# Kernel tuning notes

Measured on AMD Instinct MI355X. Metric: run time of the kernel, lower is better.

The kernel has to match this reference:

```python
import jax, jax.numpy as jnp
import numpy as np

B, N, C = 4, 4096, 64
TARGET = 560.0          # target_size
MIN_BOX = 5.0           # min_box_size
IOU_THR = 0.2
CONF_THR = 0.001
BOX_CONF_THR = 0.01
MAX_WH = 4096.0         # class-offset trick for class-aware NMS (YOLO-style)


def setup_inputs() -> dict:
    key = jax.random.key(0)
    k1, k2, k3, k4 = jax.random.split(key, 4)
    # proposals as xyxy boxes inside the (560,560) image, realistic sizes
    cxcy = jax.random.uniform(k1, (B, N, 2), dtype=jnp.float32) * TARGET
    wh = jax.random.uniform(k2, (B, N, 2), dtype=jnp.float32) * 100.0 + 2.0
    boxes = jnp.concatenate([cxcy - wh / 2, cxcy + wh / 2], axis=-1)  # [B,N,4]
    box_scores = jax.random.uniform(k3, (B, N), dtype=jnp.float32)    # objectness/10
    cls_preds = jax.random.uniform(k4, (B, N, C), dtype=jnp.float32)  # classifier scores
    return {"boxes": boxes, "box_scores": box_scores, "cls_preds": cls_preds}


def _pairwise_iou(b):
    # b: [N,4] xyxy -> [N,N] IoU
    area = (b[:, 2] - b[:, 0]) * (b[:, 3] - b[:, 1])
    lt = jnp.maximum(b[:, None, :2], b[None, :, :2])
    rb = jnp.minimum(b[:, None, 2:], b[None, :, 2:])
    wh = jnp.clip(rb - lt, 0.0)
    inter = wh[..., 0] * wh[..., 1]
    return inter / (area[:, None] + area[None, :] - inter + 1e-9)


def _detect_single(boxes, box_scores, cls_preds):
    # --- filter_boxes: clip to image, drop tiny boxes and low objectness ---
    b = jnp.clip(boxes, 0.0, TARGET)                       # [N,4]
    w = b[:, 2] - b[:, 0]
    h = b[:, 3] - b[:, 1]
    # YOLO-style combined confidence: objectness * per-class score
    cls_conf = cls_preds * box_scores[:, None]             # [N,C]
    conf = jnp.max(cls_conf, axis=-1)                      # [N]
    cls = jnp.argmax(cls_conf, axis=-1)                    # [N] int
    valid = ((box_scores > BOX_CONF_THR) & (w > MIN_BOX) & (h > MIN_BOX)
             & (conf > CONF_THR))
    # --- sort by confidence, descending (invalid boxes sink to bottom) ---
    score_key = jnp.where(valid, conf, -1.0)
    order = jnp.argsort(-score_key)
    b = b[order]; conf = conf[order]; cls = cls[order]; v = valid[order]
    # --- class-aware greedy NMS via per-class coordinate offset ---
    ob = b + (cls.astype(b.dtype) * MAX_WH)[:, None]
    iou = _pairwise_iou(ob)                                # [N,N]
    n = b.shape[0]
    idx = jnp.arange(n)

    def body(suppressed, i):
        keep_i = v[i] & (~suppressed[i])
        new_sup = suppressed | (keep_i & (iou[i] > IOU_THR) & (idx > i))
        return new_sup, keep_i

    _, keeps = jax.lax.scan(body, jnp.zeros(n, dtype=bool), idx)
    keep = (keeps & v).astype(b.dtype)                     # [N]
    det = jnp.concatenate([b, conf[:, None], cls.astype(b.dtype)[:, None]], -1)
    return det * keep[:, None]                             # [N,6] padded with zeros


def reference(boxes, box_scores, cls_preds):
    # [B,N,6]: (x1,y1,x2,y2,conf,class) per kept detection, zero rows otherwise
    return jax.vmap(_detect_single)(boxes, box_scores, cls_preds)
```

## Files before the change

kernel.cpp:

```cpp
#include <hip/hip_runtime.h>
#include <stdint.h>

#pragma clang fp contract(off)

typedef unsigned long long u64;
typedef unsigned int u32;
typedef unsigned short u16;

namespace {
constexpr int BB = 4;
constexpr int NN = 4096;
constexpr int CC = 64;
constexpr int BN = BB * NN;
constexpr float TARGET = 560.0f;
constexpr float MIN_BOX = 5.0f;
constexpr float IOU_THR = 0.2f;
constexpr float CONF_THR = 0.001f;
constexpr float BOX_CONF_THR = 0.01f;
constexpr float MAX_WH = 4096.0f;
constexpr int MAXB = 1024;
}

__device__ __forceinline__ void zero_row(float* __restrict__ out, int p) {
    float2* o2 = (float2*)(out + (size_t)p * 6);
    float2 z; z.x = 0.0f; z.y = 0.0f;
    o2[0] = z; o2[1] = z; o2[2] = z;
}

__device__ __forceinline__ void emit_row(float* __restrict__ out, int p,
                                         float4 bc, float cf, float cls) {
    float2* o2 = (float2*)(out + (size_t)p * 6);
    float2 aa; aa.x = bc.x; aa.y = bc.y;
    float2 cc; cc.x = bc.z; cc.y = bc.w;
    float2 ee; ee.x = cf;   ee.y = cls;
    o2[0] = aa; o2[1] = cc; o2[2] = ee;
}

__device__ __forceinline__ float conf_of(u32 mm) {
    return __uint_as_float(mm & 0x7FFFFFFFu);
}

__device__ __forceinline__ bool iou_gt(float4 bi, float ai, float4 bj, float aj) {
    float ltx = fmaxf(bi.x, bj.x);
    float lty = fmaxf(bi.y, bj.y);
    float rbx = fminf(bi.z, bj.z);
    float rby = fminf(bi.w, bj.w);
    float ww = fmaxf(rbx - ltx, 0.0f);
    float hh = fmaxf(rby - lty, 0.0f);
    float inter = ww * hh;
    float iou = inter / (ai + aj - inter + 1e-9f);
    return iou > IOU_THR;
}

__global__ __launch_bounds__(256) void k1_score(const float* __restrict__ boxes,
                                                const float* __restrict__ box_scores,
                                                const float* __restrict__ cls_preds,
                                                float4* __restrict__ boxes_c,
                                                u32* __restrict__ key32,
                                                int* __restrict__ rank,
                                                u64* __restrict__ clsmask,
                                                int* __restrict__ kvb) {
    __shared__ u32 cvs[64];
    int r = (blockIdx.x << 6) + (threadIdx.x >> 2);
    int sub = threadIdx.x & 3;
    float bs = box_scores[r];
    const float4* cp = (const float4*)(cls_preds + ((size_t)r << 6) + (sub << 4));
    float best = -1.0f;
    int bestc = sub << 4;
#pragma unroll
    for (int q = 0; q < 4; ++q) {
        float4 v = cp[q];
        float p0 = v.x * bs, p1 = v.y * bs, p2 = v.z * bs, p3 = v.w * bs;
        int cb = (sub << 4) + (q << 2);
        if (p0 > best) { best = p0; bestc = cb + 0; }
        if (p1 > best) { best = p1; bestc = cb + 1; }
        if (p2 > best) { best = p2; bestc = cb + 2; }
        if (p3 > best) { best = p3; bestc = cb + 3; }
    }
#pragma unroll
    for (int d2 = 1; d2 < 4; d2 <<= 1) {
        float ob = __shfl_xor(best, d2);
        int oc = __shfl_xor(bestc, d2);
        if (ob > best || (ob == best && oc < bestc)) { best = ob; bestc = oc; }
    }
    if (sub == 0) {
        float4 bx = ((const float4*)boxes)[r];
        float x1 = fminf(fmaxf(bx.x, 0.0f), TARGET);
        float y1 = fminf(fmaxf(bx.y, 0.0f), TARGET);
        float x2 = fminf(fmaxf(bx.z, 0.0f), TARGET);
        float y2 = fminf(fmaxf(bx.w, 0.0f), TARGET);
        float w = x2 - x1, h = y2 - y1;
        bool valid = (bs > BOX_CONF_THR) && (w > MIN_BOX) && (h > MIN_BOX) && (best > CONF_THR);
        float sk = valid ? best : -1.0f;
        unsigned fb = __float_as_uint(sk);
        unsigned mm = (fb & 0x80000000u) ? ~fb : (fb | 0x80000000u);
        key32[r] = mm;
        float4 bc4; bc4.x = x1; bc4.y = y1; bc4.z = x2; bc4.w = y2;
        boxes_c[r] = bc4;
        rank[r] = 0;
        cvs[threadIdx.x >> 2] = (u32)bestc | (valid ? 256u : 0u);
    }
    if (threadIdx.x == 0) kvb[blockIdx.x >> 6] = 0;
    __syncthreads();
    if (threadIdx.x < 64) {
        u32 s = cvs[threadIdx.x];
        int cls = (int)(s & 255u);
        bool v = (s & 256u) != 0u;
        u64 mym = 0;
        for (int c = 0; c < 64; ++c) {
            u64 m = __ballot(v && (cls == c));
            if (threadIdx.x == c) mym = m;
        }
        int b = blockIdx.x >> 6, g = blockIdx.x & 63;
        clsmask[(((size_t)(b << 6) + (size_t)threadIdx.x) << 6) + g] = mym;
    }
}

__global__ __launch_bounds__(256) void k2_rank(const u32* __restrict__ key32,
                                               int* __restrict__ rank,
                                               int* __restrict__ kvb) {
    int bid = blockIdx.x;
    int kseg = bid & 7;
    int eseg = (bid >> 3) & 15;
    int b    = bid >> 7;
    int lane = threadIdx.x & 63;
    const u32* kb = key32 + ((size_t)b << 12);
    int i = (eseg << 8) + threadIdx.x;
    u32 my = kb[i];
    const u32* ks = kb + (kseg << 9);
    int r = 0;
    u32 kl = ks[lane];
    for (int c = 0; c < 8; ++c) {
        u32 nxt = (c < 7) ? ks[((c + 1) << 6) + lane] : 0u;
        int lim = i - ((kseg << 9) + (c << 6));
#pragma unroll
        for (int t = 0; t < 64; ++t) {
            u32 bk = __shfl(kl, t);
            r += (int)(bk > my) + (int)((bk == my) & (t < lim));
        }
        kl = nxt;
    }
    atomicAdd(&rank[(b << 12) + i], r);
    if (kseg == 0) {
        u64 bal = __ballot(my >= 0x80000000u);
        if (lane == 0) atomicAdd(&kvb[b], (int)__popcll(bal));
    }
}

__global__ __launch_bounds__(64) void k3_nms(const float4* __restrict__ boxes_c,
                                             const u32* __restrict__ key32,
                                             const int* __restrict__ rank,
                                             const u64* __restrict__ clsmask,
                                             const int* __restrict__ kvb,
                                             float* __restrict__ out) {
    __shared__ u32 bitset[128];
    __shared__ u16 pos2e[NN];
    __shared__ u16 lpos[MAXB];
    __shared__ float4 lbox[MAXB];
    const int lane = threadIdx.x;
    const int b = blockIdx.x >> 6;
    const int myc = blockIdx.x & 63;
    const int base = b << 12;
    const float off = (float)myc * MAX_WH;

    const int kv = kvb[b];
    {
        int p = kv + myc + (lane << 6);
        if (p < NN) zero_row(out, base + p);
    }

    bitset[2 * lane] = 0;
    bitset[2 * lane + 1] = 0;
    __syncthreads();

    {
        u64 m = clsmask[(((size_t)(b << 6) + (size_t)myc) << 6) + lane];
        while (m) {
            int bit = (int)__builtin_ctzll(m); m &= m - 1;
            int e = (lane << 6) + bit;
            int rk = rank[base + e];
            atomicOr(&bitset[rk >> 5], 1u << (rk & 31));
            pos2e[rk] = (u16)e;
        }
    }
    __syncthreads();

    u64 w = ((u64)bitset[2 * lane + 1] << 32) | (u64)bitset[2 * lane];
    int cnt = (int)__popcll(w);
    int incl = cnt;
#pragma unroll
    for (int d2 = 1; d2 < 64; d2 <<= 1) {
        int t2 = __shfl_up(incl, d2);
        if (lane >= d2) incl += t2;
    }
    int kk = __shfl(incl, 63);
    {
        int d = incl - cnt;
        u64 t = w;
        while (t) {
            int b2 = (int)__builtin_ctzll(t); t &= t - 1;
            int p = (lane << 6) + b2;
            if (d < MAXB) lpos[d] = (u16)p; else zero_row(out, base + p);
            d++;
        }
    }
    if (kk > MAXB) kk = MAXB;
    if (kk == 0) return;
    __syncthreads();

    if (kk <= 128) {
        const int j0 = lane, j1 = 64 + lane;
        bool in0 = j0 < kk, in1 = j1 < kk;
        float4 box0 = {0, 0, 0, 0}, box1 = {0, 0, 0, 0};
        float a0 = 0.0f, a1 = 0.0f;
        if (in0) {
            float4 bc4 = boxes_c[base + pos2e[lpos[j0]]];
            box0.x = bc4.x + off; box0.y = bc4.y + off; box0.z = bc4.z + off; box0.w = bc4.w + off;
            a0 = (box0.z - box0.x) * (box0.w - box0.y);
        }
        if (in1) {
            float4 bc4 = boxes_c[base + pos2e[lpos[j1]]];
            box1.x = bc4.x + off; box1.y = bc4.y + off; box1.z = bc4.z + off; box1.w = bc4.w + off;
            a1 = (box1.z - box1.x) * (box1.w - box1.y);
        }
        u64 r00 = 0, r10 = 0, r11 = 0;
        int k0 = kk < 64 ? kk : 64;
        for (int i = 0; i < k0; ++i) {
            float4 bi; float ai;
            bi.x = __shfl(box0.x, i); bi.y = __shfl(box0.y, i);
            bi.z = __shfl(box0.z, i); bi.w = __shfl(box0.w, i);
            ai = __shfl(a0, i);
            bool s0 = in0 && (j0 > i) && iou_gt(bi, ai, box0, a0);
            r00 |= ((u64)s0) << i;
            if (kk > 64) {
                bool s1 = in1 && iou_gt(bi, ai, box1, a1);
                r10 |= ((u64)s1) << i;
            }
        }
        for (int i = 64; i < kk; ++i) {
            float4 bi; float ai;
            bi.x = __shfl(box1.x, i - 64); bi.y = __shfl(box1.y, i - 64);
            bi.z = __shfl(box1.z, i - 64); bi.w = __shfl(box1.w, i - 64);
            ai = __shfl(a1, i - 64);
            bool s1 = in1 && (j1 > i) && iou_gt(bi, ai, box1, a1);
            r11 |= ((u64)s1) << (i - 64);
        }
        u32 sup0 = 0, sup1 = 0;
        int kc = kk < 64 ? kk : 64;
        for (int i = 0; i < kc; ++i) {
            u64 f = __ballot(sup0 != 0);
            u32 km = ((f >> i) & 1ull) ? 0u : ~0u;
            sup0 |= km & (u32)((r00 >> i) & 1ull);
            sup1 |= km & (u32)((r10 >> i) & 1ull);
        }
        for (int i = 64; i < kk; ++i) {
            u64 f = __ballot(sup1 != 0);
            u32 km = ((f >> (i - 64)) & 1ull) ? 0u : ~0u;
            sup1 |= km & (u32)((r11 >> (i - 64)) & 1ull);
        }
        if (in0) {
            int p = lpos[j0]; int e = base + pos2e[p];
            if (!sup0) emit_row(out, base + p, boxes_c[e], conf_of(key32[e]), (float)myc);
            else zero_row(out, base + p);
        }
        if (in1) {
            int p = lpos[j1]; int e = base + pos2e[p];
            if (!sup1) emit_row(out, base + p, boxes_c[e], conf_of(key32[e]), (float)myc);
            else zero_row(out, base + p);
        }
    } else {
        for (int m = lane; m < kk; m += 64) {
            float4 bc4 = boxes_c[base + pos2e[lpos[m]]];
            float4 ob; ob.x = bc4.x + off; ob.y = bc4.y + off; ob.z = bc4.z + off; ob.w = bc4.w + off;
            lbox[m] = ob;
        }
        __syncthreads();
        u64 supw = 0;
        for (int i = 0; i < kk; ++i) {
            u64 wd = __shfl(supw, i >> 6);
            if (((wd >> (i & 63)) & 1ull) == 0ull) {
                float4 bi = lbox[i];
                float ai = (bi.z - bi.x) * (bi.w - bi.y);
                for (int jb = (i + 1) & ~63; jb < kk; jb += 64) {
                    int j = jb + lane;
                    bool s = false;
                    if (j > i && j < kk) {
                        float4 bj = lbox[j];
                        float aj = (bj.z - bj.x) * (bj.w - bj.y);
                        s = iou_gt(bi, ai, bj, aj);
                    }
                    u64 m2 = __ballot(s);
                    if (lane == (jb >> 6)) supw |= m2;
                }
            }
        }
        for (int t2 = 0; t2 * 64 < kk; ++t2) {
            int m = t2 * 64 + lane;
            u64 wd = __shfl(supw, t2);
            if (m < kk) {
                int p = lpos[m]; int e = base + pos2e[p];
                if (((wd >> lane) & 1ull) == 0ull)
                    emit_row(out, base + p, boxes_c[e], conf_of(key32[e]), (float)myc);
                else zero_row(out, base + p);
            }
        }
    }
}

extern "C" void kernel_launch(void* const* d_in, const int* in_sizes, int n_in,
                              void* d_out, int out_size, void* d_ws, size_t ws_size,
                              hipStream_t stream) {
    const float* boxes      = (const float*)d_in[0];
    const float* box_scores = (const float*)d_in[1];
    const float* cls_preds  = (const float*)d_in[2];

    char* ws = (char*)d_ws;
    size_t off = 0;
    float4* boxes_c = (float4*)(ws + off); off += (size_t)BN * 16;
    u32*    key32   = (u32*)(ws + off);    off += (size_t)BN * 4;
    int*    rank    = (int*)(ws + off);    off += (size_t)BN * 4;
    u64*    clsmask = (u64*)(ws + off);    off += (size_t)BB * 64 * CC * 8;
    int*    kvb     = (int*)(ws + off);    off += (size_t)BB * 4;

    k1_score<<<BN / 64, 256, 0, stream>>>(boxes, box_scores, cls_preds,
                                          boxes_c, key32, rank, clsmask, kvb);
    k2_rank<<<BB * 128, 256, 0, stream>>>(key32, rank, kvb);
    k3_nms<<<BB * CC, 64, 0, stream>>>(boxes_c, key32, rank, clsmask, kvb, (float*)d_out);
}
```

Measured before the change: 117.5 us.

## Pack index into 64-bit sort key, stage rank keys in LDS, drop clipped-box buffer

```diff
diff --git a/kernel.cpp b/kernel.cpp
--- a/kernel.cpp
+++ b/kernel.cpp
@@ -36,8 +36,17 @@
     o2[0] = aa; o2[1] = cc; o2[2] = ee;
 }
 
-__device__ __forceinline__ float conf_of(u32 mm) {
-    return __uint_as_float(mm & 0x7FFFFFFFu);
+__device__ __forceinline__ float4 clip_box(float4 bx) {
+    float4 r;
+    r.x = fminf(fmaxf(bx.x, 0.0f), TARGET);
+    r.y = fminf(fmaxf(bx.y, 0.0f), TARGET);
+    r.z = fminf(fmaxf(bx.z, 0.0f), TARGET);
+    r.w = fminf(fmaxf(bx.w, 0.0f), TARGET);
+    return r;
+}
+
+__device__ __forceinline__ float conf_of(u64 key) {
+    return __uint_as_float(((u32)(key >> 12)) & 0x7FFFFFFFu);
 }
 
 __device__ __forceinline__ bool iou_gt(float4 bi, float ai, float4 bj, float aj) {
@@ -55,8 +64,7 @@
 __global__ __launch_bounds__(256) void k1_score(const float* __restrict__ boxes,
                                                 const float* __restrict__ box_scores,
                                                 const float* __restrict__ cls_preds,
-                                                float4* __restrict__ boxes_c,
-                                                u32* __restrict__ key32,
+                                                u64* __restrict__ key64,
                                                 int* __restrict__ rank,
                                                 u64* __restrict__ clsmask,
                                                 int* __restrict__ kvb) {
@@ -84,19 +92,14 @@
         if (ob > best || (ob == best && oc < bestc)) { best = ob; bestc = oc; }
     }
     if (sub == 0) {
-        float4 bx = ((const float4*)boxes)[r];
-        float x1 = fminf(fmaxf(bx.x, 0.0f), TARGET);
-        float y1 = fminf(fmaxf(bx.y, 0.0f), TARGET);
-        float x2 = fminf(fmaxf(bx.z, 0.0f), TARGET);
-        float y2 = fminf(fmaxf(bx.w, 0.0f), TARGET);
-        float w = x2 - x1, h = y2 - y1;
+        float4 bc4 = clip_box(((const float4*)boxes)[r]);
+        float w = bc4.z - bc4.x, h = bc4.w - bc4.y;
         bool valid = (bs > BOX_CONF_THR) && (w > MIN_BOX) && (h > MIN_BOX) && (best > CONF_THR);
         float sk = valid ? best : -1.0f;
         unsigned fb = __float_as_uint(sk);
         unsigned mm = (fb & 0x80000000u) ? ~fb : (fb | 0x80000000u);
-        key32[r] = mm;
-        float4 bc4; bc4.x = x1; bc4.y = y1; bc4.z = x2; bc4.w = y2;
-        boxes_c[r] = bc4;
+        int i = r & (NN - 1);
+        key64[r] = ((u64)mm << 12) | (u64)(NN - 1 - i);
         rank[r] = 0;
         cvs[threadIdx.x >> 2] = (u32)bestc | (valid ? 256u : 0u);
     }
@@ -116,39 +119,36 @@
     }
 }
 
-__global__ __launch_bounds__(256) void k2_rank(const u32* __restrict__ key32,
+__global__ __launch_bounds__(256) void k2_rank(const u64* __restrict__ key64,
                                                int* __restrict__ rank,
                                                int* __restrict__ kvb) {
+    __shared__ u64 sk[512];
     int bid = blockIdx.x;
     int kseg = bid & 7;
     int eseg = (bid >> 3) & 15;
     int b    = bid >> 7;
-    int lane = threadIdx.x & 63;
-    const u32* kb = key32 + ((size_t)b << 12);
-    int i = (eseg << 8) + threadIdx.x;
-    u32 my = kb[i];
-    const u32* ks = kb + (kseg << 9);
+    int tid = threadIdx.x;
+    const u64* kb = key64 + ((size_t)b << 12);
+    for (int p = tid; p < 512; p += 256) sk[p] = kb[(kseg << 9) + p];
+    __syncthreads();
+    int i = (eseg << 8) + tid;
+    u64 my = kb[i];
     int r = 0;
-    u32 kl = ks[lane];
-    for (int c = 0; c < 8; ++c) {
-        u32 nxt = (c < 7) ? ks[((c + 1) << 6) + lane] : 0u;
-        int lim = i - ((kseg << 9) + (c << 6));
-#pragma unroll
-        for (int t = 0; t < 64; ++t) {
-            u32 bk = __shfl(kl, t);
-            r += (int)(bk > my) + (int)((bk == my) & (t < lim));
-        }
-        kl = nxt;
+    const ulonglong2* s2 = (const ulonglong2*)sk;
+#pragma unroll 16
+    for (int q = 0; q < 256; ++q) {
+        ulonglong2 v = s2[q];
+        r += (int)(v.x > my) + (int)(v.y > my);
     }
     atomicAdd(&rank[(b << 12) + i], r);
     if (kseg == 0) {
-        u64 bal = __ballot(my >= 0x80000000u);
-        if (lane == 0) atomicAdd(&kvb[b], (int)__popcll(bal));
-    }
-}
-
-__global__ __launch_bounds__(64) void k3_nms(const float4* __restrict__ boxes_c,
-                                             const u32* __restrict__ key32,
+        u64 bal = __ballot(my >= (1ull << 43));
+        if ((tid & 63) == 0) atomicAdd(&kvb[b], (int)__popcll(bal));
+    }
+}
+
+__global__ __launch_bounds__(64) void k3_nms(const float* __restrict__ boxes,
+                                             const u64* __restrict__ key64,
                                              const int* __restrict__ rank,
                                              const u64* __restrict__ clsmask,
                                              const int* __restrict__ kvb,
@@ -157,11 +157,13 @@
     __shared__ u16 pos2e[NN];
     __shared__ u16 lpos[MAXB];
     __shared__ float4 lbox[MAXB];
+    __shared__ float larea[128];
     const int lane = threadIdx.x;
     const int b = blockIdx.x >> 6;
     const int myc = blockIdx.x & 63;
     const int base = b << 12;
     const float off = (float)myc * MAX_WH;
+    const float4* braw = (const float4*)boxes + base;
 
     const int kv = kvb[b];
     {
@@ -211,39 +213,42 @@
     if (kk <= 128) {
         const int j0 = lane, j1 = 64 + lane;
         bool in0 = j0 < kk, in1 = j1 < kk;
+        float4 bcl0 = {0, 0, 0, 0}, bcl1 = {0, 0, 0, 0};
         float4 box0 = {0, 0, 0, 0}, box1 = {0, 0, 0, 0};
         float a0 = 0.0f, a1 = 0.0f;
+        int e0 = 0, e1 = 0;
         if (in0) {
-            float4 bc4 = boxes_c[base + pos2e[lpos[j0]]];
-            box0.x = bc4.x + off; box0.y = bc4.y + off; box0.z = bc4.z + off; box0.w = bc4.w + off;
+            e0 = pos2e[lpos[j0]];
+            bcl0 = clip_box(braw[e0]);
+            box0.x = bcl0.x + off; box0.y = bcl0.y + off; box0.z = bcl0.z + off; box0.w = bcl0.w + off;
             a0 = (box0.z - box0.x) * (box0.w - box0.y);
+            lbox[j0] = box0; larea[j0] = a0;
         }
         if (in1) {
-            float4 bc4 = boxes_c[base + pos2e[lpos[j1]]];
-            box1.x = bc4.x + off; box1.y = bc4.y + off; box1.z = bc4.z + off; box1.w = bc4.w + off;
+            e1 = pos2e[lpos[j1]];
+            bcl1 = clip_box(braw[e1]);
+            box1.x = bcl1.x + off; box1.y = bcl1.y + off; box1.z = bcl1.z + off; box1.w = bcl1.w + off;
             a1 = (box1.z - box1.x) * (box1.w - box1.y);
-        }
+            lbox[j1] = box1; larea[j1] = a1;
+        }
+        __syncthreads();
         u64 r00 = 0, r10 = 0, r11 = 0;
-        int k0 = kk < 64 ? kk : 64;
-        for (int i = 0; i < k0; ++i) {
-            float4 bi; float ai;
-            bi.x = __shfl(box0.x, i); bi.y = __shfl(box0.y, i);
-            bi.z = __shfl(box0.z, i); bi.w = __shfl(box0.w, i);
-            ai = __shfl(a0, i);
-            bool s0 = in0 && (j0 > i) && iou_gt(bi, ai, box0, a0);
-            r00 |= ((u64)s0) << i;
-            if (kk > 64) {
-                bool s1 = in1 && iou_gt(bi, ai, box1, a1);
-                r10 |= ((u64)s1) << i;
+        if (kk <= 64) {
+            for (int i = 0; i < kk; ++i) {
+                float4 bi = lbox[i];
+                float ai = larea[i];
+                bool s0 = in0 && (j0 > i) && iou_gt(bi, ai, box0, a0);
+                r00 |= ((u64)s0) << i;
             }
-        }
-        for (int i = 64; i < kk; ++i) {
-            float4 bi; float ai;
-            bi.x = __shfl(box1.x, i - 64); bi.y = __shfl(box1.y, i - 64);
-            bi.z = __shfl(box1.z, i - 64); bi.w = __shfl(box1.w, i - 64);
-            ai = __shfl(a1, i - 64);
-            bool s1 = in1 && (j1 > i) && iou_gt(bi, ai, box1, a1);
-            r11 |= ((u64)s1) << (i - 64);
+        } else {
+            for (int i = 0; i < kk; ++i) {
+                float4 bi = lbox[i];
+                float ai = larea[i];
+                bool s0 = in0 && (j0 > i) && iou_gt(bi, ai, box0, a0);
+                bool s1 = in1 && (j1 > i) && iou_gt(bi, ai, box1, a1);
+                if (i < 64) { r00 |= ((u64)s0) << i; r10 |= ((u64)s1) << i; }
+                else        { r11 |= ((u64)s1) << (i - 64); }
+            }
         }
         u32 sup0 = 0, sup1 = 0;
         int kc = kk < 64 ? kk : 64;
@@ -259,18 +264,18 @@
             sup1 |= km & (u32)((r11 >> (i - 64)) & 1ull);
         }
         if (in0) {
-            int p = lpos[j0]; int e = base + pos2e[p];
-            if (!sup0) emit_row(out, base + p, boxes_c[e], conf_of(key32[e]), (float)myc);
+            int p = lpos[j0];
+            if (!sup0) emit_row(out, base + p, bcl0, conf_of(key64[base + e0]), (float)myc);
             else zero_row(out, base + p);
         }
         if (in1) {
-            int p = lpos[j1]; int e = base + pos2e[p];
-            if (!sup1) emit_row(out, base + p, boxes_c[e], conf_of(key32[e]), (float)myc);
+            int p = lpos[j1];
+            if (!sup1) emit_row(out, base + p, bcl1, conf_of(key64[base + e1]), (float)myc);
             else zero_row(out, base + p);
         }
     } else {
         for (int m = lane; m < kk; m += 64) {
-            float4 bc4 = boxes_c[base + pos2e[lpos[m]]];
+            float4 bc4 = clip_box(braw[pos2e[lpos[m]]]);
             float4 ob; ob.x = bc4.x + off; ob.y = bc4.y + off; ob.z = bc4.z + off; ob.w = bc4.w + off;
             lbox[m] = ob;
         }
@@ -298,10 +303,11 @@
             int m = t2 * 64 + lane;
             u64 wd = __shfl(supw, t2);
             if (m < kk) {
-                int p = lpos[m]; int e = base + pos2e[p];
-                if (((wd >> lane) & 1ull) == 0ull)
-                    emit_row(out, base + p, boxes_c[e], conf_of(key32[e]), (float)myc);
-                else zero_row(out, base + p);
+                int p = lpos[m]; int e = pos2e[p];
+                if (((wd >> lane) & 1ull) == 0ull) {
+                    float4 bc4 = clip_box(braw[e]);
+                    emit_row(out, base + p, bc4, conf_of(key64[base + e]), (float)myc);
+                } else zero_row(out, base + p);
             }
         }
     }
@@ -316,14 +322,13 @@
 
     char* ws = (char*)d_ws;
     size_t off = 0;
-    float4* boxes_c = (float4*)(ws + off); off += (size_t)BN * 16;
-    u32*    key32   = (u32*)(ws + off);    off += (size_t)BN * 4;
-    int*    rank    = (int*)(ws + off);    off += (size_t)BN * 4;
-    u64*    clsmask = (u64*)(ws + off);    off += (size_t)BB * 64 * CC * 8;
-    int*    kvb     = (int*)(ws + off);    off += (size_t)BB * 4;
+    u64* key64   = (u64*)(ws + off); off += (size_t)BN * 8;
+    int* rank    = (int*)(ws + off); off += (size_t)BN * 4;
+    u64* clsmask = (u64*)(ws + off); off += (size_t)BB * 64 * CC * 8;
+    int* kvb     = (int*)(ws + off); off += (size_t)BB * 4;
 
     k1_score<<<BN / 64, 256, 0, stream>>>(boxes, box_scores, cls_preds,
-                                          boxes_c, key32, rank, clsmask, kvb);
-    k2_rank<<<BB * 128, 256, 0, stream>>>(key32, rank, kvb);
-    k3_nms<<<BB * CC, 64, 0, stream>>>(boxes_c, key32, rank, clsmask, kvb, (float*)d_out);
-}
+                                          key64, rank, clsmask, kvb);
+    k2_rank<<<BB * 128, 256, 0, stream>>>(key64, rank, kvb);
+    k3_nms<<<BB * CC, 64, 0, stream>>>(boxes, key64, rank, clsmask, kvb, (float*)d_out);
+}
```

New measurement: 99.27 us. -15.5%, faster.
